# Kernel optimization log

Hardware: AMD Instinct MI355X
Metric: run time of the kernel (lower is better)

Reference implementation:

```python
import jax, jax.numpy as jnp
import numpy as np

N = 50000   # nodes
E = 800000  # edges
D = 64      # dim_node
H = 64      # hidden_channels
G = 512     # graphs in batch


def setup_inputs() -> dict:
    key = jax.random.key(0)
    ks = jax.random.split(key, 13)
    s = 0.05
    return dict(
        x=jax.random.normal(ks[0], (N, D), jnp.float32),
        edge_index=jax.random.randint(ks[1], (2, E), 0, N, dtype=jnp.int32),
        batch_idx=jnp.sort(jax.random.randint(ks[2], (N,), 0, G, dtype=jnp.int32)),
        W0=jax.random.normal(ks[3], (D, H), jnp.float32) * s,
        b0=jnp.zeros((H,), jnp.float32),
        W1=jax.random.normal(ks[4], (H, H), jnp.float32) * s,
        b1=jnp.zeros((H,), jnp.float32),
        W2=jax.random.normal(ks[5], (H, H), jnp.float32) * s,
        b2=jnp.zeros((H,), jnp.float32),
        lin1_w=jax.random.normal(ks[6], (H, H), jnp.float32) * s,
        lin1_b=jnp.zeros((H,), jnp.float32),
        lin2_w=jax.random.normal(ks[7], (H, 1), jnp.float32) * s,
        lin2_b=jnp.zeros((1,), jnp.float32),
    )


def gcn_conv(x, W, b, src, dst, n):
    """PyG GCNConv: out = D^{-1/2} (A + I) D^{-1/2} X W + b (self-loops added)."""
    h = x @ W                                   # [n, H] transform first (cheaper)
    loop = jnp.arange(n, dtype=src.dtype)
    row = jnp.concatenate([src, loop])          # message sources (incl. self-loops)
    col = jnp.concatenate([dst, loop])          # aggregation targets
    deg = jax.ops.segment_sum(jnp.ones_like(col, jnp.float32), col, num_segments=n)
    dinv = jnp.where(deg > 0, jax.lax.rsqrt(deg), 0.0)
    norm = dinv[row] * dinv[col]                # [E+n]
    msg = h[row] * norm[:, None]                # gather + scale
    return jax.ops.segment_sum(msg, col, num_segments=n) + b


def reference(x, edge_index, batch_idx, W0, b0, W1, b1, W2, b2,
              lin1_w, lin1_b, lin2_w, lin2_b):
    src, dst = edge_index[0], edge_index[1]
    h = jax.nn.relu(gcn_conv(x, W0, b0, src, dst, N))   # dropout(p=0, eval) = identity
    h = jax.nn.relu(gcn_conv(h, W1, b1, src, dst, N))
    h = jax.nn.relu(gcn_conv(h, W2, b2, src, dst, N))
    # global_mean_pool over graph ids
    sums = jax.ops.segment_sum(h, batch_idx, num_segments=G)            # [G, H]
    cnt = jax.ops.segment_sum(jnp.ones((N,), jnp.float32), batch_idx, num_segments=G)
    pooled = sums / jnp.maximum(cnt, 1.0)[:, None]
    h = jax.nn.relu(pooled @ lin1_w + lin1_b)
    return h @ lin2_w + lin2_b                                          # [G, 1]
```

## Files before the change

kernel.cpp:

```cpp
#include <hip/hip_runtime.h>
#include <math.h>

#define NN 50000
#define EE 800000
#define HH 64
#define GG 512
#define SCAN_NB ((NN + 1023) / 1024)

typedef unsigned short ushort_t;
typedef unsigned int uint_t;

__device__ __forceinline__ ushort_t f32_to_bf16(float f) {
    uint_t u = __float_as_uint(f);
    uint_t bias = 0x7FFFu + ((u >> 16) & 1u);
    return (ushort_t)((u + bias) >> 16);
}
__device__ __forceinline__ float bf16_to_f32(ushort_t h) {
    return __uint_as_float(((uint_t)h) << 16);
}


__global__ void k_deg(const int* __restrict__ dst, int* __restrict__ deg,
                      int* __restrict__ rank) {
    int e = blockIdx.x * blockDim.x + threadIdx.x;
    if (e < EE) rank[e] = atomicAdd(&deg[dst[e]], 1);
}


__global__ void __launch_bounds__(1024) k_scan1(const int* __restrict__ deg,
                                                int* __restrict__ rowptr,
                                                int* __restrict__ bsum,
                                                float* __restrict__ dinv) {
    int tid = threadIdx.x;
    int lane = tid & 63, w = tid >> 6;
    int i = blockIdx.x * 1024 + tid;
    int v = (i < NN) ? deg[i] : 0;
    if (i < NN)       dinv[i] = 1.0f / sqrtf((float)(v + 1));
    else if (i == NN) dinv[i] = 0.0f;
    int x = v;
#pragma unroll
    for (int off = 1; off < 64; off <<= 1) {
        int y = __shfl_up(x, off);
        if (lane >= off) x += y;
    }
    __shared__ int ws[16];
    if (lane == 63) ws[w] = x;
    __syncthreads();
    if (tid < 16) {
        int y = ws[tid];
        int z = y;
#pragma unroll
        for (int off = 1; off < 16; off <<= 1) {
            int t2 = __shfl_up(z, off);
            if (tid >= off) z += t2;
        }
        ws[tid] = z - y;
    }
    __syncthreads();
    int excl = x - v + ws[w];
    if (i <= NN) rowptr[i] = excl;
    if (tid == 1023) bsum[blockIdx.x] = excl + v;
}

__global__ void __launch_bounds__(64) k_scan2(int* __restrict__ bsum) {
    int lane = threadIdx.x;
    int v = (lane < SCAN_NB) ? bsum[lane] : 0;
    int x = v;
#pragma unroll
    for (int off = 1; off < 64; off <<= 1) {
        int y = __shfl_up(x, off);
        if (lane >= off) x += y;
    }
    if (lane < SCAN_NB) bsum[lane] = x - v;
}


__global__ void k_fill(const int* __restrict__ src, const int* __restrict__ dst,
                       const int* __restrict__ rank,
                       const int* __restrict__ rowptr, const int* __restrict__ bsum,
                       const int* __restrict__ batch,
                       ushort_t* __restrict__ csr_src, int* __restrict__ cnt) {
    int tid = blockIdx.x * blockDim.x + threadIdx.x;
    if (tid < EE) {
        int d = dst[tid];
        csr_src[rowptr[d] + bsum[d >> 10] + rank[tid]] = (ushort_t)src[tid];
    } else if (tid < EE + NN) {
        atomicAdd(&cnt[batch[tid - EE]], 1);
    }
}


template<bool RELU>
__global__ void __launch_bounds__(256) k_xform(const float* __restrict__ x,
                                               const float* __restrict__ W,
                                               const float* __restrict__ dinv,
                                               ushort_t* __restrict__ t) {
    __shared__ float sW[64 * 64];
    __shared__ float sX[32 * 65];
    int tid = threadIdx.x;
    for (int k = tid; k < 64 * 64; k += 256) sW[k] = W[k];
    int row0 = blockIdx.x * 32;
    for (int v = tid; v < 32 * 16; v += 256) {
        int r  = v >> 4;
        int k4 = (v & 15) * 4;
        int row = row0 + r;
        float4 val = make_float4(0.f, 0.f, 0.f, 0.f);
        if (row < NN) val = *(const float4*)(x + (size_t)row * 64 + k4);
        if (RELU) {
            val.x = fmaxf(val.x, 0.f); val.y = fmaxf(val.y, 0.f);
            val.z = fmaxf(val.z, 0.f); val.w = fmaxf(val.w, 0.f);
        }
        sX[r * 65 + k4 + 0] = val.x;
        sX[r * 65 + k4 + 1] = val.y;
        sX[r * 65 + k4 + 2] = val.z;
        sX[r * 65 + k4 + 3] = val.w;
    }
    __syncthreads();
    int r  = tid >> 3;
    int c0 = (tid & 7) * 8;
    float acc[8] = {0.f, 0.f, 0.f, 0.f, 0.f, 0.f, 0.f, 0.f};
    for (int k = 0; k < 64; ++k) {
        float xv = sX[r * 65 + k];
#pragma unroll
        for (int j = 0; j < 8; ++j) acc[j] = fmaf(xv, sW[k * 64 + c0 + j], acc[j]);
    }
    int row = row0 + r;
    if (row <= NN) {
        float dv = dinv[row];
        uint_t pk[4];
#pragma unroll
        for (int j = 0; j < 4; ++j) {
            ushort_t lo = f32_to_bf16(acc[2 * j] * dv);
            ushort_t hi = f32_to_bf16(acc[2 * j + 1] * dv);
            pk[j] = (uint_t)lo | ((uint_t)hi << 16);
        }
        uint4* o = (uint4*)(t + (size_t)row * 64 + c0);
        *o = make_uint4(pk[0], pk[1], pk[2], pk[3]);
    }
}


template<bool POOL>
__global__ void __launch_bounds__(256) k_gather(const ushort_t* __restrict__ t,
                                                const float* __restrict__ dinv,
                                                const int* __restrict__ rowptr,
                                                const int* __restrict__ bsum,
                                                const ushort_t* __restrict__ csr_src,
                                                const float* __restrict__ b,
                                                const int* __restrict__ batch,
                                                float* __restrict__ out) {
    int i = __builtin_amdgcn_readfirstlane((blockIdx.x * blockDim.x + threadIdx.x) >> 6);
    int c = threadIdx.x & 63;
    if (i >= NN) return;
    int e   = __builtin_amdgcn_readfirstlane(rowptr[i]     + bsum[i >> 10]);
    int end = __builtin_amdgcn_readfirstlane(rowptr[i + 1] + bsum[(i + 1) >> 10]);
    float acc = bf16_to_f32(t[(size_t)i * 64 + c]);
    float a0 = 0.f, a1 = 0.f, a2 = 0.f, a3 = 0.f;
    for (; e < end; e += 16) {
        int s[16];
#pragma unroll
        for (int j = 0; j < 16; ++j) {
            int sj = (int)csr_src[e + j];
            s[j] = (e + j < end) ? sj : NN;
        }
        ushort_t v[16];
#pragma unroll
        for (int j = 0; j < 16; ++j) v[j] = t[(size_t)s[j] * 64 + c];
#pragma unroll
        for (int j = 0; j < 16; ++j) {
            float f = bf16_to_f32(v[j]);
            if ((j & 3) == 0)      a0 += f;
            else if ((j & 3) == 1) a1 += f;
            else if ((j & 3) == 2) a2 += f;
            else                   a3 += f;
        }
    }
    acc += (a0 + a1) + (a2 + a3);
    float r = fmaf(acc, dinv[i], b[c]);
    if (POOL) {
        atomicAdd(&out[(size_t)batch[i] * 64 + c], fmaxf(r, 0.0f));
    } else {
        out[(size_t)i * 64 + c] = r;
    }
}


__global__ void __launch_bounds__(64) k_head(const float* __restrict__ pooled,
                                             const int* __restrict__ cnt,
                                             const float* __restrict__ w1,
                                             const float* __restrict__ b1,
                                             const float* __restrict__ w2,
                                             const float* __restrict__ b2,
                                             float* __restrict__ out) {
    int g = blockIdx.x;
    int c = threadIdx.x;
    __shared__ float sp[64];
    float cf = fmaxf((float)cnt[g], 1.0f);
    sp[c] = pooled[(size_t)g * 64 + c] / cf;
    __syncthreads();
    float acc = b1[c];
    for (int k = 0; k < 64; ++k) acc = fmaf(sp[k], w1[k * 64 + c], acc);
    float h1 = fmaxf(acc, 0.0f);
    float p = h1 * w2[c];
#pragma unroll
    for (int off = 32; off > 0; off >>= 1) p += __shfl_down(p, off);
    if (c == 0) out[g] = p + b2[0];
}


extern "C" void kernel_launch(void* const* d_in, const int* in_sizes, int n_in,
                              void* d_out, int out_size, void* d_ws, size_t ws_size,
                              hipStream_t stream) {
    const float* x      = (const float*)d_in[0];
    const int*   ei     = (const int*)d_in[1];
    const int*   batch  = (const int*)d_in[2];
    const float* W0     = (const float*)d_in[3];
    const float* b0     = (const float*)d_in[4];
    const float* W1     = (const float*)d_in[5];
    const float* b1     = (const float*)d_in[6];
    const float* W2     = (const float*)d_in[7];
    const float* b2     = (const float*)d_in[8];
    const float* lin1w  = (const float*)d_in[9];
    const float* lin1b  = (const float*)d_in[10];
    const float* lin2w  = (const float*)d_in[11];
    const float* lin2b  = (const float*)d_in[12];
    float* out = (float*)d_out;

    const int* src = ei;
    const int* dst = ei + EE;

    char* ws = (char*)d_ws;
    size_t off = 0;
    auto carve = [&](size_t bytes) {
        void* p = ws + off;
        off = (off + bytes + 255) & ~(size_t)255;
        return p;
    };
    int*      deg      = (int*)carve((size_t)NN * 4);
    float*    pooled   = (float*)carve((size_t)GG * 64 * 4);
    int*      cnt      = (int*)carve((size_t)GG * 4);
    size_t zero_span = off;
    float*    dinv     = (float*)carve((size_t)(NN + 1) * 4);
    int*      rowptr   = (int*)carve((size_t)(NN + 1) * 4);
    int*      bsum     = (int*)carve((size_t)SCAN_NB * 4);
    int*      rank     = (int*)carve((size_t)EE * 4);
    ushort_t* csr_src  = (ushort_t*)carve((size_t)(EE + 16) * 2);
    ushort_t* bufT     = (ushort_t*)carve((size_t)(NN + 1) * 64 * 2);
    float*    bufA     = (float*)carve((size_t)NN * 64 * 4);

    hipMemsetAsync(deg, 0, zero_span, stream);

    k_deg  <<<(EE + 255) / 256, 256, 0, stream>>>(dst, deg, rank);
    k_scan1<<<SCAN_NB, 1024, 0, stream>>>(deg, rowptr, bsum, dinv);
    k_scan2<<<1, 64, 0, stream>>>(bsum);
    k_fill <<<(EE + NN + 255) / 256, 256, 0, stream>>>(src, dst, rank, rowptr,
                                                       bsum, batch, csr_src, cnt);

    const int xgrid = (NN + 1 + 31) / 32;
    const int ggrid = (NN * 64) / 256;

    k_xform<false><<<xgrid, 256, 0, stream>>>(x, W0, dinv, bufT);
    k_gather<false><<<ggrid, 256, 0, stream>>>(bufT, dinv, rowptr, bsum, csr_src,
                                               b0, batch, bufA);
    k_xform<true><<<xgrid, 256, 0, stream>>>(bufA, W1, dinv, bufT);
    k_gather<false><<<ggrid, 256, 0, stream>>>(bufT, dinv, rowptr, bsum, csr_src,
                                               b1, batch, bufA);
    k_xform<true><<<xgrid, 256, 0, stream>>>(bufA, W2, dinv, bufT);
    k_gather<true><<<ggrid, 256, 0, stream>>>(bufT, dinv, rowptr, bsum, csr_src,
                                              b2, batch, pooled);

    k_head<<<GG, 64, 0, stream>>>(pooled, cnt, lin1w, lin1b, lin2w, lin2b, out);
}
```

Measured before the change: 319.8 us.

## Split degree atomics into eight sub-counters and precompute absolute row pointers

Degree counting now spreads atomics over eight replicated counter arrays, chosen by edge block, so fewer edges contend on the same address. The scan sums the copies and stores packed 16-bit per-copy offsets. A new kernel turns these into absolute per-copy bases and absolute row pointers, so the fill and gather kernels no longer add the block sums. This costs extra memory traffic for the larger counter, offset and base arrays, plus one more kernel launch.

```diff
diff --git a/kernel.cpp b/kernel.cpp
--- a/kernel.cpp
+++ b/kernel.cpp
@@ -6,6 +6,7 @@
 #define HH 64
 #define GG 512
 #define SCAN_NB ((NN + 1023) / 1024)
+#define NC 8
 
 typedef unsigned short ushort_t;
 typedef unsigned int uint_t;
@@ -20,23 +21,42 @@
 }
 
 
-__global__ void k_deg(const int* __restrict__ dst, int* __restrict__ deg,
+__global__ void k_deg(const int* __restrict__ dst, int* __restrict__ degc,
                       int* __restrict__ rank) {
     int e = blockIdx.x * blockDim.x + threadIdx.x;
-    if (e < EE) rank[e] = atomicAdd(&deg[dst[e]], 1);
-}
-
-
-__global__ void __launch_bounds__(1024) k_scan1(const int* __restrict__ deg,
+    if (e < EE) {
+        int c = (e >> 8) & (NC - 1);
+        rank[e] = atomicAdd(&degc[c * NN + dst[e]], 1);
+    }
+}
+
+
+__global__ void __launch_bounds__(1024) k_scan1(const int* __restrict__ degc,
                                                 int* __restrict__ rowptr,
                                                 int* __restrict__ bsum,
+                                                uint4* __restrict__ off8,
                                                 float* __restrict__ dinv) {
     int tid = threadIdx.x;
     int lane = tid & 63, w = tid >> 6;
     int i = blockIdx.x * 1024 + tid;
-    int v = (i < NN) ? deg[i] : 0;
-    if (i < NN)       dinv[i] = 1.0f / sqrtf((float)(v + 1));
-    else if (i == NN) dinv[i] = 0.0f;
+    int total = 0;
+    int offv[NC];
+#pragma unroll
+    for (int c = 0; c < NC; ++c) {
+        int dc = (i < NN) ? degc[c * NN + i] : 0;
+        offv[c] = total;
+        total += dc;
+    }
+    if (i < NN) {
+        dinv[i] = 1.0f / sqrtf((float)(total + 1));
+        off8[i] = make_uint4((uint_t)offv[0] | ((uint_t)offv[1] << 16),
+                             (uint_t)offv[2] | ((uint_t)offv[3] << 16),
+                             (uint_t)offv[4] | ((uint_t)offv[5] << 16),
+                             (uint_t)offv[6] | ((uint_t)offv[7] << 16));
+    } else if (i == NN) {
+        dinv[i] = 0.0f;
+    }
+    int v = (i < NN) ? total : 0;
     int x = v;
 #pragma unroll
     for (int off = 1; off < 64; off <<= 1) {
@@ -75,15 +95,36 @@
 }
 
 
+__global__ void k_base(const int* __restrict__ rowptr, const int* __restrict__ bsum,
+                       const uint4* __restrict__ off8,
+                       int* __restrict__ rowptr_abs, int* __restrict__ base8) {
+    int i = blockIdx.x * blockDim.x + threadIdx.x;
+    if (i > NN) return;
+    int base = rowptr[i] + bsum[i >> 10];
+    rowptr_abs[i] = base;
+    if (i < NN) {
+        uint4 pk = off8[i];
+        base8[0 * NN + i] = base + (int)(pk.x & 0xFFFFu);
+        base8[1 * NN + i] = base + (int)(pk.x >> 16);
+        base8[2 * NN + i] = base + (int)(pk.y & 0xFFFFu);
+        base8[3 * NN + i] = base + (int)(pk.y >> 16);
+        base8[4 * NN + i] = base + (int)(pk.z & 0xFFFFu);
+        base8[5 * NN + i] = base + (int)(pk.z >> 16);
+        base8[6 * NN + i] = base + (int)(pk.w & 0xFFFFu);
+        base8[7 * NN + i] = base + (int)(pk.w >> 16);
+    }
+}
+
+
 __global__ void k_fill(const int* __restrict__ src, const int* __restrict__ dst,
-                       const int* __restrict__ rank,
-                       const int* __restrict__ rowptr, const int* __restrict__ bsum,
+                       const int* __restrict__ rank, const int* __restrict__ base8,
                        const int* __restrict__ batch,
                        ushort_t* __restrict__ csr_src, int* __restrict__ cnt) {
     int tid = blockIdx.x * blockDim.x + threadIdx.x;
     if (tid < EE) {
         int d = dst[tid];
-        csr_src[rowptr[d] + bsum[d >> 10] + rank[tid]] = (ushort_t)src[tid];
+        int c = (tid >> 8) & (NC - 1);
+        csr_src[base8[c * NN + d] + rank[tid]] = (ushort_t)src[tid];
     } else if (tid < EE + NN) {
         atomicAdd(&cnt[batch[tid - EE]], 1);
     }
@@ -143,8 +184,7 @@
 template<bool POOL>
 __global__ void __launch_bounds__(256) k_gather(const ushort_t* __restrict__ t,
                                                 const float* __restrict__ dinv,
-                                                const int* __restrict__ rowptr,
-                                                const int* __restrict__ bsum,
+                                                const int* __restrict__ rowptr_abs,
                                                 const ushort_t* __restrict__ csr_src,
                                                 const float* __restrict__ b,
                                                 const int* __restrict__ batch,
@@ -152,8 +192,8 @@
     int i = __builtin_amdgcn_readfirstlane((blockIdx.x * blockDim.x + threadIdx.x) >> 6);
     int c = threadIdx.x & 63;
     if (i >= NN) return;
-    int e   = __builtin_amdgcn_readfirstlane(rowptr[i]     + bsum[i >> 10]);
-    int end = __builtin_amdgcn_readfirstlane(rowptr[i + 1] + bsum[(i + 1) >> 10]);
+    int e   = __builtin_amdgcn_readfirstlane(rowptr_abs[i]);
+    int end = __builtin_amdgcn_readfirstlane(rowptr_abs[i + 1]);
     float acc = bf16_to_f32(t[(size_t)i * 64 + c]);
     float a0 = 0.f, a1 = 0.f, a2 = 0.f, a3 = 0.f;
     for (; e < end; e += 16) {
@@ -236,37 +276,41 @@
         off = (off + bytes + 255) & ~(size_t)255;
         return p;
     };
-    int*      deg      = (int*)carve((size_t)NN * 4);
+    int*      degc     = (int*)carve((size_t)NC * NN * 4);
     float*    pooled   = (float*)carve((size_t)GG * 64 * 4);
     int*      cnt      = (int*)carve((size_t)GG * 4);
     size_t zero_span = off;
     float*    dinv     = (float*)carve((size_t)(NN + 1) * 4);
     int*      rowptr   = (int*)carve((size_t)(NN + 1) * 4);
     int*      bsum     = (int*)carve((size_t)SCAN_NB * 4);
+    uint4*    off8     = (uint4*)carve((size_t)NN * 16);
+    int*      rowptr_abs = (int*)carve((size_t)(NN + 1) * 4);
+    int*      base8    = (int*)carve((size_t)NC * NN * 4);
     int*      rank     = (int*)carve((size_t)EE * 4);
     ushort_t* csr_src  = (ushort_t*)carve((size_t)(EE + 16) * 2);
     ushort_t* bufT     = (ushort_t*)carve((size_t)(NN + 1) * 64 * 2);
     float*    bufA     = (float*)carve((size_t)NN * 64 * 4);
 
-    hipMemsetAsync(deg, 0, zero_span, stream);
-
-    k_deg  <<<(EE + 255) / 256, 256, 0, stream>>>(dst, deg, rank);
-    k_scan1<<<SCAN_NB, 1024, 0, stream>>>(deg, rowptr, bsum, dinv);
+    hipMemsetAsync(degc, 0, zero_span, stream);
+
+    k_deg  <<<EE / 256, 256, 0, stream>>>(dst, degc, rank);
+    k_scan1<<<SCAN_NB, 1024, 0, stream>>>(degc, rowptr, bsum, off8, dinv);
     k_scan2<<<1, 64, 0, stream>>>(bsum);
-    k_fill <<<(EE + NN + 255) / 256, 256, 0, stream>>>(src, dst, rank, rowptr,
-                                                       bsum, batch, csr_src, cnt);
+    k_base <<<(NN + 256) / 256, 256, 0, stream>>>(rowptr, bsum, off8, rowptr_abs, base8);
+    k_fill <<<(EE + NN + 255) / 256, 256, 0, stream>>>(src, dst, rank, base8,
+                                                       batch, csr_src, cnt);
 
     const int xgrid = (NN + 1 + 31) / 32;
     const int ggrid = (NN * 64) / 256;
 
     k_xform<false><<<xgrid, 256, 0, stream>>>(x, W0, dinv, bufT);
-    k_gather<false><<<ggrid, 256, 0, stream>>>(bufT, dinv, rowptr, bsum, csr_src,
+    k_gather<false><<<ggrid, 256, 0, stream>>>(bufT, dinv, rowptr_abs, csr_src,
                                                b0, batch, bufA);
     k_xform<true><<<xgrid, 256, 0, stream>>>(bufA, W1, dinv, bufT);
-    k_gather<false><<<ggrid, 256, 0, stream>>>(bufT, dinv, rowptr, bsum, csr_src,
+    k_gather<false><<<ggrid, 256, 0, stream>>>(bufT, dinv, rowptr_abs, csr_src,
                                                b1, batch, bufA);
     k_xform<true><<<xgrid, 256, 0, stream>>>(bufA, W2, dinv, bufT);
-    k_gather<true><<<ggrid, 256, 0, stream>>>(bufT, dinv, rowptr, bsum, csr_src,
+    k_gather<true><<<ggrid, 256, 0, stream>>>(bufT, dinv, rowptr_abs, csr_src,
                                               b2, batch, pooled);
 
     k_head<<<GG, 64, 0, stream>>>(pooled, cnt, lin1w, lin1b, lin2w, lin2b, out);
```

Result: no change. 320.5 us (+0.2%).
